# Kernel optimization log

Hardware: AMD Instinct MI355X
Metric: run time of the kernel (lower is better)

## Reference

```python
import jax, jax.numpy as jnp
import numpy as np

B, C, T, H = 256, 8, 512, 512  # batch, channels(6 arms + 2 time), timesteps, hidden
OUT = 2


def setup_inputs() -> dict:
    key = jax.random.key(0)
    ks = jax.random.split(key, 8)
    # arm lengths positive and away from 0 (denominator 0.15*arm in likelihood)
    arms = jax.random.uniform(ks[0], (B, 6, T), minval=0.5, maxval=1.5)
    tm = jax.random.uniform(ks[1], (B, 2, T))
    inputs = jnp.concatenate([arms, tm], axis=1)  # (B, 8, T)
    s_in = 1.0 / np.sqrt(6.0)
    s_rec = 1.0 / np.sqrt(float(H))
    W_in = jax.random.uniform(ks[2], (H, 6), minval=-s_in, maxval=s_in)
    b_in = jax.random.uniform(ks[3], (H,), minval=-s_in, maxval=s_in)
    W_rec = jax.random.uniform(ks[4], (H, H), minval=-s_rec, maxval=s_rec)
    b_rec = jax.random.uniform(ks[5], (H,), minval=-s_rec, maxval=s_rec)
    W_key = jax.random.uniform(ks[6], (OUT, H), minval=-s_rec, maxval=s_rec)
    b_key = jax.random.uniform(ks[7], (OUT,), minval=-s_rec, maxval=s_rec)
    return {"inputs": inputs, "W_in": W_in, "b_in": b_in,
            "W_rec": W_rec, "b_rec": b_rec, "W_key": W_key, "b_key": b_key}


def _likelihood(tm, arms):
    # tm: (B,), arms: (B, n) -> squared normalized timing mismatch; zero rows where tm==0
    prs = jnp.square((tm[:, None] - arms) / (0.15 * arms))
    return jnp.where(tm[:, None] == 0, 0.0, prs)


def reference(inputs, W_in, b_in, W_rec, b_rec, W_key, b_key):
    Bn, Cn, Tn = inputs.shape
    Hn = W_rec.shape[0]
    xs = jnp.transpose(inputs, (2, 0, 1))[1:]  # (T-1, B, 8); loop starts at t=1
    key0 = jnp.ones((Bn,), dtype=inputs.dtype)
    h0 = jnp.zeros((Bn, Hn), dtype=inputs.dtype)

    def step(carry, x_t):
        key_h_pre, h_pre = carry
        arms_pri = x_t[:, :2]
        arms_sec = x_t[:, 2:6]
        tm = x_t[:, 6:8]
        # gate secondary arms by previous key
        arms_sum = arms_sec[:, :2] * key_h_pre[:, None] + arms_sec[:, 2:] * (1.0 - key_h_pre)[:, None]
        prs_t = jnp.concatenate([_likelihood(tm[:, 0], arms_pri),
                                 _likelihood(tm[:, 1], arms_sum)], axis=1)  # (B, 4)
        inp_t = jnp.concatenate([arms_pri, arms_sum, tm], axis=1)  # (B, 6)
        h_t = jnp.tanh(inp_t @ W_in.T + b_in + h_pre @ W_rec.T + b_rec)  # (B, H)
        key_t = jax.nn.sigmoid(h_t @ W_key.T + b_key)  # (B, 2)
        return (key_t[:, 0], h_t), (key_t, prs_t, h_t)

    _, (keys, prs, hs) = jax.lax.scan(step, (key0, h0), xs)
    # prepend the t=0 zero slice and move time to last axis, matching torch buffers
    keys = jnp.concatenate([jnp.zeros((1, Bn, OUT), keys.dtype), keys], axis=0).transpose(1, 2, 0)
    prs = jnp.concatenate([jnp.zeros((1, Bn, 2 * OUT), prs.dtype), prs], axis=0).transpose(1, 2, 0)
    hs = jnp.concatenate([jnp.zeros((1, Bn, Hn), hs.dtype), hs], axis=0).transpose(1, 2, 0)
    tm_modified = inputs[:, -2:, :]
    return keys, prs, hs, tm_modified
```

## Files before the change

### kernel.cpp

```cpp
#include <hip/hip_runtime.h>

#define TDS 512
#define NBATCH 256

typedef _Float16 h2 __attribute__((ext_vector_type(2)));

__device__ __forceinline__ unsigned int pack2(float lo, float hi) {
    h2 v;
    v.x = (_Float16)lo;
    v.y = (_Float16)hi;
    return __builtin_bit_cast(unsigned int, v);
}
__device__ __forceinline__ h2 uph(unsigned int u) {
    return __builtin_bit_cast(h2, u);
}

#if __has_builtin(__builtin_amdgcn_fdot2)
__device__ __forceinline__ float fdot2(h2 w, h2 x, float acc) {
    return __builtin_amdgcn_fdot2(w, x, acc, false);
}
#else
__device__ __forceinline__ float fdot2(h2 w, h2 x, float acc) {
    return fmaf((float)w.x, (float)x.x, fmaf((float)w.y, (float)x.y, acc));
}
#endif

__device__ __forceinline__ float fast_rcp(float x) {
#if __has_builtin(__builtin_amdgcn_rcpf)
    return __builtin_amdgcn_rcpf(x);
#else
    return 1.0f / x;
#endif
}

__device__ __forceinline__ float fast_tanh(float x) {
    return 1.0f - 2.0f * fast_rcp(1.0f + __expf(2.0f * x));
}
__device__ __forceinline__ float fast_sigmoid(float x) {
    return fast_rcp(1.0f + __expf(-x));
}

#define KEYS_OFF 0u
#define PRS_OFF  262144u
#define HS_OFF   786432u
#define TM_OFF   67895296u

#define HP_CHUNK 72
#define HP_BUF   (4 * HP_CHUNK)

__device__ __forceinline__ void flush_window(
    float* __restrict__ g_out, int b, int tid, int w,
    const float* __restrict__ lds_hst,
    const float (*__restrict__ kst)[2],
    const float (*__restrict__ pst)[4],
    float k0loc, float k1loc)
{
    const int tbase = w * 8;
    float h[8];
#pragma unroll
    for (int s = 0; s < 8; ++s) h[s] = lds_hst[s * TDS + tid];
    float4* dst = (float4*)(g_out + HS_OFF + (unsigned)b * 262144u + (unsigned)tid * 512u + (unsigned)tbase);
    dst[0] = make_float4(h[0], h[1], h[2], h[3]);
    dst[1] = make_float4(h[4], h[5], h[6], h[7]);

    if (tid < 2) {
        float k[8];
#pragma unroll
        for (int s = 0; s < 7; ++s) k[s] = kst[s][tid];
        k[7] = (tid == 0) ? k0loc : k1loc;
        float4* kd = (float4*)(g_out + KEYS_OFF + (unsigned)b * 1024u + (unsigned)tid * 512u + (unsigned)tbase);
        kd[0] = make_float4(k[0], k[1], k[2], k[3]);
        kd[1] = make_float4(k[4], k[5], k[6], k[7]);
    } else if (tid < 6) {
        const int o = tid - 2;
        float p[8];
#pragma unroll
        for (int s = 0; s < 8; ++s) p[s] = pst[s][o];
        float4* pd = (float4*)(g_out + PRS_OFF + (unsigned)b * 2048u + (unsigned)o * 512u + (unsigned)tbase);
        pd[0] = make_float4(p[0], p[1], p[2], p[3]);
        pd[1] = make_float4(p[4], p[5], p[6], p[7]);
    }
}

__global__ __launch_bounds__(TDS, 1) void rnn_att_kernel(
    const float* __restrict__ g_inputs,
    const float* __restrict__ g_Win,
    const float* __restrict__ g_bin,
    const float* __restrict__ g_Wrec,
    const float* __restrict__ g_brec,
    const float* __restrict__ g_Wkey,
    const float* __restrict__ g_bkey,
    float* __restrict__ g_out)
{
    __shared__ __attribute__((aligned(16))) unsigned int lds_w[64][TDS];
    __shared__ __attribute__((aligned(16))) unsigned int lds_hp[2 * HP_BUF];
    __shared__ __attribute__((aligned(16))) float lds_hst[8 * TDS];
    __shared__ __attribute__((aligned(16))) float lds_ksum[2][16];
    __shared__ float lds_kst[2][8][2];
    __shared__ float lds_pst[2][8][4];

    const int tid = threadIdx.x;
    const int b = blockIdx.x;
    const int kc = tid & 3;
    const int rg = tid >> 2;
    const int r_out = tid;

    unsigned int wreg[192];
#pragma unroll
    for (int i = 0; i < 4; ++i) {
        const int r = (rg << 2) + i;
        const float4* src = (const float4*)(g_Wrec + r * 512 + kc * 128);
#pragma unroll
        for (int g = 0; g < 16; ++g) {
            float4 f0 = src[2 * g];
            float4 f1 = src[2 * g + 1];
            unsigned int u0 = pack2(f0.x, f0.y);
            unsigned int u1 = pack2(f0.z, f0.w);
            unsigned int u2 = pack2(f1.x, f1.y);
            unsigned int u3 = pack2(f1.z, f1.w);
            if (g < 12) {
                wreg[i * 48 + g * 4 + 0] = u0;
                wreg[i * 48 + g * 4 + 1] = u1;
                wreg[i * 48 + g * 4 + 2] = u2;
                wreg[i * 48 + g * 4 + 3] = u3;
            } else {
                const int pbase = i * 16 + (g - 12) * 4;
                lds_w[pbase + 0][tid] = u0;
                lds_w[pbase + 1][tid] = u1;
                lds_w[pbase + 2][tid] = u2;
                lds_w[pbase + 3][tid] = u3;
            }
        }
    }

    float win[6];
#pragma unroll
    for (int j = 0; j < 6; ++j) win[j] = g_Win[r_out * 6 + j];
    const float bias = g_bin[r_out] + g_brec[r_out];
    const float wk0 = g_Wkey[r_out];
    const float wk1 = g_Wkey[512 + r_out];
    const float bk0 = g_bkey[0];
    const float bk1 = g_bkey[1];

    lds_hp[tid] = 0u;
    if (tid < 2 * HP_BUF - TDS) lds_hp[TDS + tid] = 0u;

    if (tid < 256) {
        const float4* s = (const float4*)(g_inputs + b * 4096 + 3072);
        float4* d = (float4*)(g_out + TM_OFF + (unsigned)b * 1024u);
        d[tid] = s[tid];
    }

    lds_hst[tid] = 0.0f;
    if (tid == 0) {
        lds_pst[0][0][0] = 0.0f; lds_pst[0][0][1] = 0.0f;
        lds_pst[0][0][2] = 0.0f; lds_pst[0][0][3] = 0.0f;
        lds_kst[0][0][0] = 0.0f; lds_kst[0][0][1] = 0.0f;
    }
    __syncthreads();

    const float* gin = g_inputs + b * 4096;
    float key_pre = 1.0f;
    float xv[8];
#pragma unroll
    for (int j = 0; j < 8; ++j) xv[j] = gin[512 * j + 1];

    for (int t = 1; t < 512; ++t) {
        __syncthreads();

        float k0 = 0.0f, k1 = 0.0f;
        if (t > 1) {
            const float4* ks = (const float4*)&lds_ksum[(t - 1) & 1][0];
            float4 v0 = ks[0], v1 = ks[1], v2 = ks[2], v3 = ks[3];
            float s0 = ((v0.x + v1.x) + (v2.x + v3.x)) + ((v0.z + v1.z) + (v2.z + v3.z));
            float s1 = ((v0.y + v1.y) + (v2.y + v3.y)) + ((v0.w + v1.w) + (v2.w + v3.w));
            k0 = fast_sigmoid(s0 + bk0);
            k1 = fast_sigmoid(s1 + bk1);
            key_pre = k0;
            if (tid == 0) {
                const int slot = (t - 1) & 7;
                const int par = ((t - 1) >> 3) & 1;
                lds_kst[par][slot][0] = k0;
                lds_kst[par][slot][1] = k1;
            }
        }

        if ((t & 7) == 0) {
            const int w = (t >> 3) - 1;
            flush_window(g_out, b, tid, w, lds_hst, lds_kst[w & 1], lds_pst[w & 1], k0, k1);
        }

        float xn[8];
        {
            const int tn = (t < 511) ? t + 1 : 511;
#pragma unroll
            for (int j = 0; j < 8; ++j) xn[j] = gin[512 * j + tn];
        }

        const float x0 = xv[0], x1 = xv[1], x2 = xv[2], x3 = xv[3];
        const float x4 = xv[4], x5 = xv[5], x6 = xv[6], x7 = xv[7];
        float wd = bias;
        wd = fmaf(x0, win[0], wd);
        wd = fmaf(x1, win[1], wd);
        wd = fmaf(x4, win[2], wd);
        wd = fmaf(x5, win[3], wd);
        wd = fmaf(x6, win[4], wd);
        wd = fmaf(x7, win[5], wd);
        const float wdk = (x2 - x4) * win[2] + (x3 - x5) * win[3];
        wd = fmaf(key_pre, wdk, wd);

        const unsigned int* hb = lds_hp + ((t - 1) & 1) * HP_BUF + kc * HP_CHUNK;
        float a[4] = {0.0f, 0.0f, 0.0f, 0.0f};
#pragma unroll
        for (int c = 0; c < 12; ++c) {
            uint4 hu = ((const uint4*)hb)[c];
            h2 x0h = uph(hu.x), x1h = uph(hu.y), x2h = uph(hu.z), x3h = uph(hu.w);
#pragma unroll
            for (int i = 0; i < 4; ++i) {
                a[i] = fdot2(uph(wreg[i * 48 + 4 * c + 0]), x0h, a[i]);
                a[i] = fdot2(uph(wreg[i * 48 + 4 * c + 1]), x1h, a[i]);
                a[i] = fdot2(uph(wreg[i * 48 + 4 * c + 2]), x2h, a[i]);
                a[i] = fdot2(uph(wreg[i * 48 + 4 * c + 3]), x3h, a[i]);
            }
        }
#pragma unroll
        for (int c = 0; c < 4; ++c) {
            uint4 hu = ((const uint4*)(hb + 48))[c];
            h2 x0h = uph(hu.x), x1h = uph(hu.y), x2h = uph(hu.z), x3h = uph(hu.w);
#pragma unroll
            for (int i = 0; i < 4; ++i) {
                a[i] = fdot2(uph(lds_w[i * 16 + 4 * c + 0][tid]), x0h, a[i]);
                a[i] = fdot2(uph(lds_w[i * 16 + 4 * c + 1][tid]), x1h, a[i]);
                a[i] = fdot2(uph(lds_w[i * 16 + 4 * c + 2][tid]), x2h, a[i]);
                a[i] = fdot2(uph(lds_w[i * 16 + 4 * c + 3][tid]), x3h, a[i]);
            }
        }
#pragma unroll
        for (int i = 0; i < 4; ++i) {
            a[i] += __shfl_xor(a[i], 1, 64);
            a[i] += __shfl_xor(a[i], 2, 64);
        }
        float rsum = a[0];
        if (kc == 1) rsum = a[1];
        if (kc == 2) rsum = a[2];
        if (kc == 3) rsum = a[3];
        const float h_new = fast_tanh(rsum + wd);

        const float h_other = __shfl_xor(h_new, 1, 64);
        if ((tid & 1) == 0) {
            const int p = tid >> 1;
            lds_hp[(t & 1) * HP_BUF + (p >> 6) * HP_CHUNK + (p & 63)] = pack2(h_new, h_other);
        }
        lds_hst[(t & 7) * TDS + r_out] = h_new;

        float kp0 = h_new * wk0, kp1 = h_new * wk1;
#pragma unroll
        for (int m = 1; m < 64; m <<= 1) {
            kp0 += __shfl_xor(kp0, m, 64);
            kp1 += __shfl_xor(kp1, m, 64);
        }
        if ((tid & 63) == 0) {
            lds_ksum[t & 1][(tid >> 6) * 2 + 0] = kp0;
            lds_ksum[t & 1][(tid >> 6) * 2 + 1] = kp1;
        }

        if (tid == 0) {
            const float as0 = fmaf(key_pre, x2 - x4, x4);
            const float as1 = fmaf(key_pre, x3 - x5, x5);
            const float q0 = (x6 - x0) * fast_rcp(0.15f * x0);
            const float q1 = (x6 - x1) * fast_rcp(0.15f * x1);
            const float q2 = (x7 - as0) * fast_rcp(0.15f * as0);
            const float q3 = (x7 - as1) * fast_rcp(0.15f * as1);
            float p0 = q0 * q0, p1 = q1 * q1, p2 = q2 * q2, p3 = q3 * q3;
            if (x6 == 0.0f) { p0 = 0.0f; p1 = 0.0f; }
            if (x7 == 0.0f) { p2 = 0.0f; p3 = 0.0f; }
            const int par = (t >> 3) & 1;
            lds_pst[par][t & 7][0] = p0;
            lds_pst[par][t & 7][1] = p1;
            lds_pst[par][t & 7][2] = p2;
            lds_pst[par][t & 7][3] = p3;
        }

#pragma unroll
        for (int j = 0; j < 8; ++j) xv[j] = xn[j];
    }

    __syncthreads();
    float k0, k1;
    {
        const float4* ks = (const float4*)&lds_ksum[1][0];
        float4 v0 = ks[0], v1 = ks[1], v2 = ks[2], v3 = ks[3];
        float s0 = ((v0.x + v1.x) + (v2.x + v3.x)) + ((v0.z + v1.z) + (v2.z + v3.z));
        float s1 = ((v0.y + v1.y) + (v2.y + v3.y)) + ((v0.w + v1.w) + (v2.w + v3.w));
        k0 = fast_sigmoid(s0 + bk0);
        k1 = fast_sigmoid(s1 + bk1);
    }
    flush_window(g_out, b, tid, 63, lds_hst, lds_kst[1], lds_pst[1], k0, k1);
}

extern "C" void kernel_launch(void* const* d_in, const int* in_sizes, int n_in,
                              void* d_out, int out_size, void* d_ws, size_t ws_size,
                              hipStream_t stream) {
    rnn_att_kernel<<<dim3(NBATCH), dim3(TDS), 0, stream>>>(
        (const float*)d_in[0],
        (const float*)d_in[1],
        (const float*)d_in[2],
        (const float*)d_in[3],
        (const float*)d_in[4],
        (const float*)d_in[5],
        (const float*)d_in[6],
        (float*)d_out);
}
```

Baseline: 2.016 ms.

## Use DPP reductions, fp16 hidden staging, and flush outputs every 16 steps

```diff
diff --git a/kernel.cpp b/kernel.cpp
--- a/kernel.cpp
+++ b/kernel.cpp
@@ -32,13 +32,51 @@
     return 1.0f / x;
 #endif
 }
-
 __device__ __forceinline__ float fast_tanh(float x) {
     return 1.0f - 2.0f * fast_rcp(1.0f + __expf(2.0f * x));
 }
 __device__ __forceinline__ float fast_sigmoid(float x) {
     return fast_rcp(1.0f + __expf(-x));
 }
+
+#if __has_builtin(__builtin_amdgcn_update_dpp)
+#define HAVE_DPP 1
+template <int CTRL, int RM = 0xF, int BM = 0xF, bool BC = true>
+__device__ __forceinline__ float dpp0(float v) {
+    return __builtin_bit_cast(float,
+        __builtin_amdgcn_update_dpp(0, __builtin_bit_cast(int, v), CTRL, RM, BM, BC));
+}
+__device__ __forceinline__ float quad_red_sum(float v) {
+    v += dpp0<0xB1>(v);
+    v += dpp0<0x4E>(v);
+    return v;
+}
+__device__ __forceinline__ float wave_red_sum(float v) {
+    v += dpp0<0x111>(v);
+    v += dpp0<0x112>(v);
+    v += dpp0<0x114>(v);
+    v += dpp0<0x118>(v);
+    v += dpp0<0x142, 0xA>(v);
+    v += dpp0<0x143, 0xC>(v);
+    return v;
+}
+__device__ __forceinline__ float pair_swap(float v) {
+    return dpp0<0xB1>(v);
+}
+#else
+#define HAVE_DPP 0
+__device__ __forceinline__ float quad_red_sum(float v) {
+    v += __shfl_xor(v, 1, 64);
+    v += __shfl_xor(v, 2, 64);
+    return v;
+}
+__device__ __forceinline__ float wave_red_sum(float v) {
+#pragma unroll
+    for (int m = 1; m < 64; m <<= 1) v += __shfl_xor(v, m, 64);
+    return v;
+}
+__device__ __forceinline__ float pair_swap(float v) { return __shfl_xor(v, 1, 64); }
+#endif
 
 #define KEYS_OFF 0u
 #define PRS_OFF  262144u
@@ -50,35 +88,39 @@
 
 __device__ __forceinline__ void flush_window(
     float* __restrict__ g_out, int b, int tid, int w,
-    const float* __restrict__ lds_hst,
+    const unsigned int (*__restrict__ hsth)[256],
     const float (*__restrict__ kst)[2],
-    const float (*__restrict__ pst)[4],
-    float k0loc, float k1loc)
+    const float (*__restrict__ pst)[4])
 {
-    const int tbase = w * 8;
-    float h[8];
-#pragma unroll
-    for (int s = 0; s < 8; ++s) h[s] = lds_hst[s * TDS + tid];
-    float4* dst = (float4*)(g_out + HS_OFF + (unsigned)b * 262144u + (unsigned)tid * 512u + (unsigned)tbase);
-    dst[0] = make_float4(h[0], h[1], h[2], h[3]);
-    dst[1] = make_float4(h[4], h[5], h[6], h[7]);
+    const unsigned tbase = (unsigned)w * 16u;
+    float h[16];
+#pragma unroll
+    for (int s = 0; s < 16; ++s) {
+        h2 hp = uph(hsth[s][tid >> 1]);
+        h[s] = (tid & 1) ? (float)hp.y : (float)hp.x;
+    }
+    float4* dst = (float4*)(g_out + HS_OFF + (unsigned)b * 262144u + (unsigned)tid * 512u + tbase);
+#pragma unroll
+    for (int g = 0; g < 4; ++g)
+        dst[g] = make_float4(h[4 * g], h[4 * g + 1], h[4 * g + 2], h[4 * g + 3]);
 
     if (tid < 2) {
-        float k[8];
-#pragma unroll
-        for (int s = 0; s < 7; ++s) k[s] = kst[s][tid];
-        k[7] = (tid == 0) ? k0loc : k1loc;
-        float4* kd = (float4*)(g_out + KEYS_OFF + (unsigned)b * 1024u + (unsigned)tid * 512u + (unsigned)tbase);
-        kd[0] = make_float4(k[0], k[1], k[2], k[3]);
-        kd[1] = make_float4(k[4], k[5], k[6], k[7]);
+        float k[16];
+#pragma unroll
+        for (int s = 0; s < 16; ++s) k[s] = kst[s][tid];
+        float4* kd = (float4*)(g_out + KEYS_OFF + (unsigned)b * 1024u + (unsigned)tid * 512u + tbase);
+#pragma unroll
+        for (int g = 0; g < 4; ++g)
+            kd[g] = make_float4(k[4 * g], k[4 * g + 1], k[4 * g + 2], k[4 * g + 3]);
     } else if (tid < 6) {
         const int o = tid - 2;
-        float p[8];
-#pragma unroll
-        for (int s = 0; s < 8; ++s) p[s] = pst[s][o];
-        float4* pd = (float4*)(g_out + PRS_OFF + (unsigned)b * 2048u + (unsigned)o * 512u + (unsigned)tbase);
-        pd[0] = make_float4(p[0], p[1], p[2], p[3]);
-        pd[1] = make_float4(p[4], p[5], p[6], p[7]);
+        float p[16];
+#pragma unroll
+        for (int s = 0; s < 16; ++s) p[s] = pst[s][o];
+        float4* pd = (float4*)(g_out + PRS_OFF + (unsigned)b * 2048u + (unsigned)o * 512u + tbase);
+#pragma unroll
+        for (int g = 0; g < 4; ++g)
+            pd[g] = make_float4(p[4 * g], p[4 * g + 1], p[4 * g + 2], p[4 * g + 3]);
     }
 }
 
@@ -94,10 +136,10 @@
 {
     __shared__ __attribute__((aligned(16))) unsigned int lds_w[64][TDS];
     __shared__ __attribute__((aligned(16))) unsigned int lds_hp[2 * HP_BUF];
-    __shared__ __attribute__((aligned(16))) float lds_hst[8 * TDS];
+    __shared__ __attribute__((aligned(16))) unsigned int lds_hsth[16][256];
     __shared__ __attribute__((aligned(16))) float lds_ksum[2][16];
-    __shared__ float lds_kst[2][8][2];
-    __shared__ float lds_pst[2][8][4];
+    __shared__ float lds_kst[16][2];
+    __shared__ float lds_pst[16][4];
 
     const int tid = threadIdx.x;
     const int b = blockIdx.x;
@@ -151,11 +193,10 @@
         d[tid] = s[tid];
     }
 
-    lds_hst[tid] = 0.0f;
+    if (tid < 256) lds_hsth[0][tid] = 0u;
     if (tid == 0) {
-        lds_pst[0][0][0] = 0.0f; lds_pst[0][0][1] = 0.0f;
-        lds_pst[0][0][2] = 0.0f; lds_pst[0][0][3] = 0.0f;
-        lds_kst[0][0][0] = 0.0f; lds_kst[0][0][1] = 0.0f;
+        lds_pst[0][0] = 0.0f; lds_pst[0][1] = 0.0f; lds_pst[0][2] = 0.0f; lds_pst[0][3] = 0.0f;
+        lds_kst[0][0] = 0.0f; lds_kst[0][1] = 0.0f;
     }
     __syncthreads();
 
@@ -166,28 +207,10 @@
     for (int j = 0; j < 8; ++j) xv[j] = gin[512 * j + 1];
 
     for (int t = 1; t < 512; ++t) {
-        __syncthreads();
-
-        float k0 = 0.0f, k1 = 0.0f;
-        if (t > 1) {
-            const float4* ks = (const float4*)&lds_ksum[(t - 1) & 1][0];
-            float4 v0 = ks[0], v1 = ks[1], v2 = ks[2], v3 = ks[3];
-            float s0 = ((v0.x + v1.x) + (v2.x + v3.x)) + ((v0.z + v1.z) + (v2.z + v3.z));
-            float s1 = ((v0.y + v1.y) + (v2.y + v3.y)) + ((v0.w + v1.w) + (v2.w + v3.w));
-            k0 = fast_sigmoid(s0 + bk0);
-            k1 = fast_sigmoid(s1 + bk1);
-            key_pre = k0;
-            if (tid == 0) {
-                const int slot = (t - 1) & 7;
-                const int par = ((t - 1) >> 3) & 1;
-                lds_kst[par][slot][0] = k0;
-                lds_kst[par][slot][1] = k1;
-            }
-        }
-
-        if ((t & 7) == 0) {
-            const int w = (t >> 3) - 1;
-            flush_window(g_out, b, tid, w, lds_hst, lds_kst[w & 1], lds_pst[w & 1], k0, k1);
+        if ((t & 15) == 0) {
+            __syncthreads();
+            flush_window(g_out, b, tid, (t >> 4) - 1, lds_hsth, lds_kst, lds_pst);
+            __syncthreads();
         }
 
         float xn[8];
@@ -236,30 +259,24 @@
             }
         }
 #pragma unroll
-        for (int i = 0; i < 4; ++i) {
-            a[i] += __shfl_xor(a[i], 1, 64);
-            a[i] += __shfl_xor(a[i], 2, 64);
-        }
+        for (int i = 0; i < 4; ++i) a[i] = quad_red_sum(a[i]);
         float rsum = a[0];
         if (kc == 1) rsum = a[1];
         if (kc == 2) rsum = a[2];
         if (kc == 3) rsum = a[3];
         const float h_new = fast_tanh(rsum + wd);
 
-        const float h_other = __shfl_xor(h_new, 1, 64);
+        const float h_other = pair_swap(h_new);
         if ((tid & 1) == 0) {
             const int p = tid >> 1;
-            lds_hp[(t & 1) * HP_BUF + (p >> 6) * HP_CHUNK + (p & 63)] = pack2(h_new, h_other);
-        }
-        lds_hst[(t & 7) * TDS + r_out] = h_new;
-
-        float kp0 = h_new * wk0, kp1 = h_new * wk1;
-#pragma unroll
-        for (int m = 1; m < 64; m <<= 1) {
-            kp0 += __shfl_xor(kp0, m, 64);
-            kp1 += __shfl_xor(kp1, m, 64);
-        }
-        if ((tid & 63) == 0) {
+            const unsigned int hpk = pack2(h_new, h_other);
+            lds_hp[(t & 1) * HP_BUF + (p >> 6) * HP_CHUNK + (p & 63)] = hpk;
+            lds_hsth[t & 15][p] = hpk;
+        }
+
+        float kp0 = wave_red_sum(h_new * wk0);
+        float kp1 = wave_red_sum(h_new * wk1);
+        if ((tid & 63) == 63) {
             lds_ksum[t & 1][(tid >> 6) * 2 + 0] = kp0;
             lds_ksum[t & 1][(tid >> 6) * 2 + 1] = kp1;
         }
@@ -274,11 +291,26 @@
             float p0 = q0 * q0, p1 = q1 * q1, p2 = q2 * q2, p3 = q3 * q3;
             if (x6 == 0.0f) { p0 = 0.0f; p1 = 0.0f; }
             if (x7 == 0.0f) { p2 = 0.0f; p3 = 0.0f; }
-            const int par = (t >> 3) & 1;
-            lds_pst[par][t & 7][0] = p0;
-            lds_pst[par][t & 7][1] = p1;
-            lds_pst[par][t & 7][2] = p2;
-            lds_pst[par][t & 7][3] = p3;
+            lds_pst[t & 15][0] = p0;
+            lds_pst[t & 15][1] = p1;
+            lds_pst[t & 15][2] = p2;
+            lds_pst[t & 15][3] = p3;
+        }
+
+        __syncthreads();
+
+        {
+            const float4* ks = (const float4*)&lds_ksum[t & 1][0];
+            float4 v0 = ks[0], v1 = ks[1], v2 = ks[2], v3 = ks[3];
+            float s0 = ((v0.x + v1.x) + (v2.x + v3.x)) + ((v0.z + v1.z) + (v2.z + v3.z));
+            float s1 = ((v0.y + v1.y) + (v2.y + v3.y)) + ((v0.w + v1.w) + (v2.w + v3.w));
+            const float k0 = fast_sigmoid(s0 + bk0);
+            const float k1 = fast_sigmoid(s1 + bk1);
+            key_pre = k0;
+            if (tid == 0) {
+                lds_kst[t & 15][0] = k0;
+                lds_kst[t & 15][1] = k1;
+            }
         }
 
 #pragma unroll
@@ -286,16 +318,7 @@
     }
 
     __syncthreads();
-    float k0, k1;
-    {
-        const float4* ks = (const float4*)&lds_ksum[1][0];
-        float4 v0 = ks[0], v1 = ks[1], v2 = ks[2], v3 = ks[3];
-        float s0 = ((v0.x + v1.x) + (v2.x + v3.x)) + ((v0.z + v1.z) + (v2.z + v3.z));
-        float s1 = ((v0.y + v1.y) + (v2.y + v3.y)) + ((v0.w + v1.w) + (v2.w + v3.w));
-        k0 = fast_sigmoid(s0 + bk0);
-        k1 = fast_sigmoid(s1 + bk1);
-    }
-    flush_window(g_out, b, tid, 63, lds_hst, lds_kst[1], lds_pst[1], k0, k1);
+    flush_window(g_out, b, tid, 31, lds_hsth, lds_kst, lds_pst);
 }
 
 extern "C" void kernel_launch(void* const* d_in, const int* in_sizes, int n_in,
```

Measured after the change: 2.260 ms. 12.1% more time.
